# Kernel tuning notes

Measured on AMD Instinct MI355X. Metric: run time of the kernel, lower is better.

The kernel has to match this reference:

```python
import jax, jax.numpy as jnp
import numpy as np

N_NODES = 100000
N_EDGES = 1600000
EDGE_OUT = 48
HID = 128
NODE_OUT = 64


def setup_inputs() -> dict:
    key = jax.random.key(0)
    ks = jax.random.split(key, 8)
    x = jax.random.normal(ks[0], (N_NODES, 16), dtype=jnp.float32)
    edge_index = jax.random.randint(ks[1], (2, N_EDGES), 0, N_NODES, dtype=jnp.int64)
    edge_attr = jax.random.normal(ks[2], (N_EDGES, EDGE_OUT), dtype=jnp.float32)
    u = jax.random.normal(ks[3], (1, 8), dtype=jnp.float32)
    batch = jnp.zeros((N_NODES,), dtype=jnp.int64)
    # MLP params: Linear(3*edge_out, hid) -> ReLU -> Linear(hid, node_out)
    s1 = 1.0 / np.sqrt(3 * EDGE_OUT)
    s2 = 1.0 / np.sqrt(HID)
    W1 = jax.random.uniform(ks[4], (3 * EDGE_OUT, HID), jnp.float32, -s1, s1)
    b1 = jax.random.uniform(ks[5], (HID,), jnp.float32, -s1, s1)
    W2 = jax.random.uniform(ks[6], (HID, NODE_OUT), jnp.float32, -s2, s2)
    b2 = jax.random.uniform(ks[7], (NODE_OUT,), jnp.float32, -s2, s2)
    return {"x": x, "edge_index": edge_index, "edge_attr": edge_attr, "u": u,
            "batch": batch, "W1": W1, "b1": b1, "W2": W2, "b2": b2}


def reference(x, edge_index, edge_attr, u, batch, W1, b1, W2, b2):
    n = x.shape[0]
    col = edge_index[1]
    # fused-style aggregations over destination node indices
    out1 = jax.ops.segment_sum(edge_attr, col, num_segments=n)                      # scatter_add
    out2 = jax.ops.segment_max(edge_attr, col, num_segments=n)                      # scatter_max
    out2 = jnp.where(jnp.isneginf(out2), jnp.zeros((), edge_attr.dtype), out2)       # empty segments -> 0 (torch_scatter)
    cnt = jax.ops.segment_sum(jnp.ones((edge_attr.shape[0], 1), edge_attr.dtype), col, num_segments=n)
    out3 = out1 / jnp.maximum(cnt, jnp.ones((), edge_attr.dtype))                    # scatter_mean
    feat = jnp.concatenate([out1, out2, out3], axis=1)                               # [n, 3*edge_out]
    h = jax.nn.relu(feat @ W1 + b1)
    return h @ W2 + b2
```

## Files before the change

kernel.cpp:

```cpp
#include <hip/hip_runtime.h>
#include <math.h>

#define N_NODES 100000
#define N_EDGES 1600000
#define EO 48
constexpr int FEAT = 3 * EO;
constexpr int K1   = 160;
constexpr int HID  = 128;
constexpr int NOUT = 64;
constexpr int MAXD = 64;
constexpr int FEAT_ROWS_ALLOC = 100048;

typedef __attribute__((ext_vector_type(8))) short short8;
typedef __attribute__((ext_vector_type(4))) float floatx4;

__device__ __forceinline__ unsigned short f2bf(float f) {
  unsigned int u = __float_as_uint(f);
  unsigned int r = (u + 0x7fffu + ((u >> 16) & 1u)) >> 16;
  return (unsigned short)r;
}

__global__ void init_prep_kernel(int* __restrict__ cursor,
                                 const float* __restrict__ W1, const float* __restrict__ W2,
                                 unsigned short* __restrict__ W1T, unsigned short* __restrict__ W2T) {
  int i = blockIdx.x * blockDim.x + threadIdx.x;
  if (i < N_NODES) cursor[i] = 0;
  if (i < HID * K1) {
    int c = i / K1, k = i - c * K1;
    W1T[i] = (k < FEAT) ? f2bf(W1[k * HID + c]) : (unsigned short)0;
  } else {
    int j = i - HID * K1;
    if (j < NOUT * HID) {
      int c = j / HID, k = j - c * HID;
      W2T[j] = f2bf(W2[k * NOUT + c]);
    }
  }
}

__global__ void scatter_slots_kernel(const int4* __restrict__ col4, int* __restrict__ cursor,
                                     int* __restrict__ slots) {
  int i = blockIdx.x * blockDim.x + threadIdx.x;
  if (i < N_EDGES / 4) {
    int4 c = col4[i];
    int e = i * 4;
    int p;
    p = atomicAdd(&cursor[c.x], 1); if (p < MAXD) slots[c.x * MAXD + p] = e;
    p = atomicAdd(&cursor[c.y], 1); if (p < MAXD) slots[c.y * MAXD + p] = e + 1;
    p = atomicAdd(&cursor[c.z], 1); if (p < MAXD) slots[c.z * MAXD + p] = e + 2;
    p = atomicAdd(&cursor[c.w], 1); if (p < MAXD) slots[c.w * MAXD + p] = e + 3;
  }
}

__launch_bounds__(256)
__global__ void gather_kernel(const float* __restrict__ ea,
                              const int* __restrict__ slots,
                              const int* __restrict__ cursor,
                              unsigned short* __restrict__ featbf) {
  const int wid  = threadIdx.x >> 6;
  const int lane = threadIdx.x & 63;
  const int g = blockIdx.x * 4 + wid;
  if (g >= N_NODES) return;

  int deg = cursor[g];
  if (deg > MAXD) deg = MAXD;
  float s = 0.0f, m = -INFINITY;

  if (deg > 0) {
    int eidv = slots[g * MAXD + (lane < deg ? lane : deg - 1)];
    int t = 0;
    for (; t + 16 <= deg; t += 16) {
      int e[16];
#pragma unroll
      for (int j = 0; j < 16; ++j) e[j] = __builtin_amdgcn_readlane(eidv, t + j);
      if (lane < EO) {
        float v[16];
#pragma unroll
        for (int j = 0; j < 16; ++j) v[j] = ea[(size_t)e[j] * EO + lane];
#pragma unroll
        for (int j = 0; j < 16; ++j) { s += v[j]; m = fmaxf(m, v[j]); }
      }
    }
    for (; t + 4 <= deg; t += 4) {
      int e0 = __builtin_amdgcn_readlane(eidv, t + 0);
      int e1 = __builtin_amdgcn_readlane(eidv, t + 1);
      int e2 = __builtin_amdgcn_readlane(eidv, t + 2);
      int e3 = __builtin_amdgcn_readlane(eidv, t + 3);
      if (lane < EO) {
        float v0 = ea[(size_t)e0 * EO + lane];
        float v1 = ea[(size_t)e1 * EO + lane];
        float v2 = ea[(size_t)e2 * EO + lane];
        float v3 = ea[(size_t)e3 * EO + lane];
        s += (v0 + v1) + (v2 + v3);
        m = fmaxf(m, fmaxf(fmaxf(v0, v1), fmaxf(v2, v3)));
      }
    }
    for (; t < deg; ++t) {
      int e0 = __builtin_amdgcn_readlane(eidv, t);
      if (lane < EO) {
        float v = ea[(size_t)e0 * EO + lane];
        s += v;
        m = fmaxf(m, v);
      }
    }
  }

  if (lane < EO) {
    if (deg == 0) m = 0.0f;
    float mean = s / (float)(deg > 0 ? deg : 1);
    unsigned short* row = featbf + (size_t)g * FEAT;
    row[lane]          = f2bf(s);
    row[EO + lane]     = f2bf(m);
    row[2 * EO + lane] = f2bf(mean);
  }
}

__launch_bounds__(256)
__global__ void mlp_kernel(const unsigned short* __restrict__ featbf,
                           const unsigned short* __restrict__ W1T,
                           const unsigned short* __restrict__ W2T,
                           const float* __restrict__ b1,
                           const float* __restrict__ b2,
                           float* __restrict__ out) {
  __shared__ unsigned short h_lds[64][HID + 8];

  const int tid  = threadIdx.x;
  const int w    = tid >> 6;
  const int lane = tid & 63;
  const int llo  = lane & 15;
  const int lhi  = lane >> 4;

  const int g0   = blockIdx.x * 64;
  int rowA = g0 + w * 16 + llo;

  floatx4 acc[8];
#pragma unroll
  for (int c = 0; c < 8; ++c) acc[c] = (floatx4)0.0f;

  const unsigned short* arow = featbf + (size_t)rowA * FEAT;
#pragma unroll
  for (int ks = 0; ks < 5; ++ks) {
    short8 afrag = *(const short8*)(arow + ks * 32 + lhi * 8);
#pragma unroll
    for (int c = 0; c < 8; ++c) {
      short8 bfrag = *(const short8*)(W1T + (size_t)(c * 16 + llo) * K1 + ks * 32 + lhi * 8);
      acc[c] = __builtin_amdgcn_mfma_f32_16x16x32_bf16(afrag, bfrag, acc[c], 0, 0, 0);
    }
  }

#pragma unroll
  for (int c = 0; c < 8; ++c) {
    int col = c * 16 + llo;
    float bias = b1[col];
#pragma unroll
    for (int r = 0; r < 4; ++r) {
      int row = w * 16 + lhi * 4 + r;
      h_lds[row][col] = f2bf(fmaxf(acc[c][r] + bias, 0.0f));
    }
  }
  __syncthreads();

  floatx4 acc2[4];
#pragma unroll
  for (int c = 0; c < 4; ++c) acc2[c] = (floatx4)0.0f;

#pragma unroll
  for (int ks = 0; ks < 4; ++ks) {
    short8 afrag = *(const short8*)&h_lds[w * 16 + llo][ks * 32 + lhi * 8];
#pragma unroll
    for (int c = 0; c < 4; ++c) {
      short8 bfrag = *(const short8*)(W2T + (size_t)(c * 16 + llo) * HID + ks * 32 + lhi * 8);
      acc2[c] = __builtin_amdgcn_mfma_f32_16x16x32_bf16(afrag, bfrag, acc2[c], 0, 0, 0);
    }
  }

#pragma unroll
  for (int c = 0; c < 4; ++c) {
    int col = c * 16 + llo;
    float bias = b2[col];
#pragma unroll
    for (int r = 0; r < 4; ++r) {
      int g = g0 + w * 16 + lhi * 4 + r;
      if (g < N_NODES) out[(size_t)g * NOUT + col] = acc2[c][r] + bias;
    }
  }
}

extern "C" void kernel_launch(void* const* d_in, const int* in_sizes, int n_in,
                              void* d_out, int out_size, void* d_ws, size_t ws_size,
                              hipStream_t stream) {
  const int*   eidx = (const int*)d_in[1];
  const float* ea   = (const float*)d_in[2];
  const float* W1   = (const float*)d_in[5];
  const float* b1   = (const float*)d_in[6];
  const float* W2   = (const float*)d_in[7];
  const float* b2   = (const float*)d_in[8];
  const int* col = eidx + N_EDGES;
  float* out = (float*)d_out;

  char* p = (char*)d_ws;
  int* cursor = (int*)p;  p += (size_t)N_NODES * 4;
  int* slots  = (int*)p;  p += (size_t)N_NODES * MAXD * 4;
  unsigned short* featbf = (unsigned short*)p;  p += (size_t)FEAT_ROWS_ALLOC * FEAT * 2;
  unsigned short* W1T = (unsigned short*)p;     p += (size_t)HID * K1 * 2;
  unsigned short* W2T = (unsigned short*)p;

  init_prep_kernel<<<(N_NODES + 255) / 256, 256, 0, stream>>>(cursor, W1, W2, W1T, W2T);
  scatter_slots_kernel<<<(N_EDGES / 4 + 255) / 256, 256, 0, stream>>>((const int4*)col, cursor, slots);
  gather_kernel<<<(N_NODES + 3) / 4, 256, 0, stream>>>(ea, slots, cursor, featbf);
  mlp_kernel<<<(N_NODES + 63) / 64, 256, 0, stream>>>(featbf, W1T, W2T, b1, b2, out);
}
```

Measured before the change: 249.7 us.

## Pre-convert edge attributes to padded fp16 and switch MLP to fp16 MFMA

Adds a conversion pass, fused into the slot-scatter kernel launch, that rewrites edge_attr from fp32 into a 64-wide padded fp16 copy. The gather kernel then reads half-width values per edge, and the feature and weight buffers plus both MFMA stages switch from bf16 to fp16. The aim is to shrink the random-access gather traffic. The trade-off is an extra full streaming read of edge_attr plus a large write of the fp16 copy on every call, and fp16 range limits on the summed features. The gather loop is also collapsed into one clamped 16-wide loop with predicated accumulation.

```diff
diff --git a/kernel.cpp b/kernel.cpp
--- a/kernel.cpp
+++ b/kernel.cpp
@@ -9,15 +9,21 @@
 constexpr int HID  = 128;
 constexpr int NOUT = 64;
 constexpr int MAXD = 64;
+constexpr int EROW = 64;
 constexpr int FEAT_ROWS_ALLOC = 100048;
+
+constexpr int SCAT_BLOCKS = (N_EDGES / 4 + 255) / 256;
+constexpr int CONV_BLOCKS = (N_EDGES * 8) / 256;
 
 typedef __attribute__((ext_vector_type(8))) short short8;
 typedef __attribute__((ext_vector_type(4))) float floatx4;
 
-__device__ __forceinline__ unsigned short f2bf(float f) {
-  unsigned int u = __float_as_uint(f);
-  unsigned int r = (u + 0x7fffu + ((u >> 16) & 1u)) >> 16;
-  return (unsigned short)r;
+__device__ __forceinline__ unsigned short f2h(float f) {
+  _Float16 h = (_Float16)f;
+  return __builtin_bit_cast(unsigned short, h);
+}
+__device__ __forceinline__ float h2f(unsigned short u) {
+  return (float)__builtin_bit_cast(_Float16, u);
 }
 
 __global__ void init_prep_kernel(int* __restrict__ cursor,
@@ -27,35 +33,54 @@
   if (i < N_NODES) cursor[i] = 0;
   if (i < HID * K1) {
     int c = i / K1, k = i - c * K1;
-    W1T[i] = (k < FEAT) ? f2bf(W1[k * HID + c]) : (unsigned short)0;
+    W1T[i] = (k < FEAT) ? f2h(W1[k * HID + c]) : (unsigned short)0;
   } else {
     int j = i - HID * K1;
     if (j < NOUT * HID) {
       int c = j / HID, k = j - c * HID;
-      W2T[j] = f2bf(W2[k * NOUT + c]);
-    }
-  }
-}
-
-__global__ void scatter_slots_kernel(const int4* __restrict__ col4, int* __restrict__ cursor,
-                                     int* __restrict__ slots) {
-  int i = blockIdx.x * blockDim.x + threadIdx.x;
-  if (i < N_EDGES / 4) {
-    int4 c = col4[i];
-    int e = i * 4;
-    int p;
-    p = atomicAdd(&cursor[c.x], 1); if (p < MAXD) slots[c.x * MAXD + p] = e;
-    p = atomicAdd(&cursor[c.y], 1); if (p < MAXD) slots[c.y * MAXD + p] = e + 1;
-    p = atomicAdd(&cursor[c.z], 1); if (p < MAXD) slots[c.z * MAXD + p] = e + 2;
-    p = atomicAdd(&cursor[c.w], 1); if (p < MAXD) slots[c.w * MAXD + p] = e + 3;
+      W2T[j] = f2h(W2[k * NOUT + c]);
+    }
+  }
+}
+
+__global__ void scatter_convert_kernel(const int4* __restrict__ col4,
+                                       int* __restrict__ cursor, int* __restrict__ slots,
+                                       const float* __restrict__ ea,
+                                       unsigned short* __restrict__ eab) {
+  const int b = blockIdx.x;
+  if (b < SCAT_BLOCKS) {
+    int i = b * 256 + threadIdx.x;
+    if (i < N_EDGES / 4) {
+      int4 c = col4[i];
+      int e = i * 4;
+      int p;
+      p = atomicAdd(&cursor[c.x], 1); if (p < MAXD) slots[c.x * MAXD + p] = e;
+      p = atomicAdd(&cursor[c.y], 1); if (p < MAXD) slots[c.y * MAXD + p] = e + 1;
+      p = atomicAdd(&cursor[c.z], 1); if (p < MAXD) slots[c.z * MAXD + p] = e + 2;
+      p = atomicAdd(&cursor[c.w], 1); if (p < MAXD) slots[c.w * MAXD + p] = e + 3;
+    }
+  } else {
+    int t = (b - SCAT_BLOCKS) * 256 + threadIdx.x;
+    int e  = t >> 3;
+    int c8 = (t & 7) * 8;
+    short8 o;
+    if (c8 < EO) {
+      const float4* p = (const float4*)(ea + (size_t)e * EO + c8);
+      float4 a = p[0], bb = p[1];
+      o[0] = f2h(a.x);  o[1] = f2h(a.y);  o[2] = f2h(a.z);  o[3] = f2h(a.w);
+      o[4] = f2h(bb.x); o[5] = f2h(bb.y); o[6] = f2h(bb.z); o[7] = f2h(bb.w);
+    } else {
+      o = (short8)0;
+    }
+    *(short8*)(eab + (size_t)e * EROW + c8) = o;
   }
 }
 
 __launch_bounds__(256)
-__global__ void gather_kernel(const float* __restrict__ ea,
+__global__ void gather_kernel(const unsigned short* __restrict__ eab,
                               const int* __restrict__ slots,
                               const int* __restrict__ cursor,
-                              unsigned short* __restrict__ featbf) {
+                              unsigned short* __restrict__ feath) {
   const int wid  = threadIdx.x >> 6;
   const int lane = threadIdx.x & 63;
   const int g = blockIdx.x * 4 + wid;
@@ -67,39 +92,18 @@
 
   if (deg > 0) {
     int eidv = slots[g * MAXD + (lane < deg ? lane : deg - 1)];
-    int t = 0;
-    for (; t + 16 <= deg; t += 16) {
-      int e[16];
-#pragma unroll
-      for (int j = 0; j < 16; ++j) e[j] = __builtin_amdgcn_readlane(eidv, t + j);
-      if (lane < EO) {
-        float v[16];
-#pragma unroll
-        for (int j = 0; j < 16; ++j) v[j] = ea[(size_t)e[j] * EO + lane];
-#pragma unroll
-        for (int j = 0; j < 16; ++j) { s += v[j]; m = fmaxf(m, v[j]); }
+    for (int t = 0; t < deg; t += 16) {
+      float v[16];
+#pragma unroll
+      for (int j = 0; j < 16; ++j) {
+        int idx = t + j;
+        if (idx >= deg) idx = deg - 1;
+        int e = __builtin_amdgcn_readlane(eidv, idx);
+        v[j] = (lane < EO) ? h2f(eab[(size_t)e * EROW + lane]) : 0.0f;
       }
-    }
-    for (; t + 4 <= deg; t += 4) {
-      int e0 = __builtin_amdgcn_readlane(eidv, t + 0);
-      int e1 = __builtin_amdgcn_readlane(eidv, t + 1);
-      int e2 = __builtin_amdgcn_readlane(eidv, t + 2);
-      int e3 = __builtin_amdgcn_readlane(eidv, t + 3);
-      if (lane < EO) {
-        float v0 = ea[(size_t)e0 * EO + lane];
-        float v1 = ea[(size_t)e1 * EO + lane];
-        float v2 = ea[(size_t)e2 * EO + lane];
-        float v3 = ea[(size_t)e3 * EO + lane];
-        s += (v0 + v1) + (v2 + v3);
-        m = fmaxf(m, fmaxf(fmaxf(v0, v1), fmaxf(v2, v3)));
-      }
-    }
-    for (; t < deg; ++t) {
-      int e0 = __builtin_amdgcn_readlane(eidv, t);
-      if (lane < EO) {
-        float v = ea[(size_t)e0 * EO + lane];
-        s += v;
-        m = fmaxf(m, v);
+#pragma unroll
+      for (int j = 0; j < 16; ++j) {
+        if (t + j < deg) { s += v[j]; m = fmaxf(m, v[j]); }
       }
     }
   }
@@ -107,15 +111,15 @@
   if (lane < EO) {
     if (deg == 0) m = 0.0f;
     float mean = s / (float)(deg > 0 ? deg : 1);
-    unsigned short* row = featbf + (size_t)g * FEAT;
-    row[lane]          = f2bf(s);
-    row[EO + lane]     = f2bf(m);
-    row[2 * EO + lane] = f2bf(mean);
+    unsigned short* row = feath + (size_t)g * FEAT;
+    row[lane]          = f2h(s);
+    row[EO + lane]     = f2h(m);
+    row[2 * EO + lane] = f2h(mean);
   }
 }
 
 __launch_bounds__(256)
-__global__ void mlp_kernel(const unsigned short* __restrict__ featbf,
+__global__ void mlp_kernel(const unsigned short* __restrict__ feath,
                            const unsigned short* __restrict__ W1T,
                            const unsigned short* __restrict__ W2T,
                            const float* __restrict__ b1,
@@ -136,14 +140,14 @@
 #pragma unroll
   for (int c = 0; c < 8; ++c) acc[c] = (floatx4)0.0f;
 
-  const unsigned short* arow = featbf + (size_t)rowA * FEAT;
+  const unsigned short* arow = feath + (size_t)rowA * FEAT;
 #pragma unroll
   for (int ks = 0; ks < 5; ++ks) {
     short8 afrag = *(const short8*)(arow + ks * 32 + lhi * 8);
 #pragma unroll
     for (int c = 0; c < 8; ++c) {
       short8 bfrag = *(const short8*)(W1T + (size_t)(c * 16 + llo) * K1 + ks * 32 + lhi * 8);
-      acc[c] = __builtin_amdgcn_mfma_f32_16x16x32_bf16(afrag, bfrag, acc[c], 0, 0, 0);
+      acc[c] = __builtin_amdgcn_mfma_f32_16x16x32_f16(afrag, bfrag, acc[c], 0, 0, 0);
     }
   }
 
@@ -154,7 +158,7 @@
 #pragma unroll
     for (int r = 0; r < 4; ++r) {
       int row = w * 16 + lhi * 4 + r;
-      h_lds[row][col] = f2bf(fmaxf(acc[c][r] + bias, 0.0f));
+      h_lds[row][col] = f2h(fmaxf(acc[c][r] + bias, 0.0f));
     }
   }
   __syncthreads();
@@ -169,7 +173,7 @@
 #pragma unroll
     for (int c = 0; c < 4; ++c) {
       short8 bfrag = *(const short8*)(W2T + (size_t)(c * 16 + llo) * HID + ks * 32 + lhi * 8);
-      acc2[c] = __builtin_amdgcn_mfma_f32_16x16x32_bf16(afrag, bfrag, acc2[c], 0, 0, 0);
+      acc2[c] = __builtin_amdgcn_mfma_f32_16x16x32_f16(afrag, bfrag, acc2[c], 0, 0, 0);
     }
   }
 
@@ -200,12 +204,14 @@
   char* p = (char*)d_ws;
   int* cursor = (int*)p;  p += (size_t)N_NODES * 4;
   int* slots  = (int*)p;  p += (size_t)N_NODES * MAXD * 4;
-  unsigned short* featbf = (unsigned short*)p;  p += (size_t)FEAT_ROWS_ALLOC * FEAT * 2;
+  unsigned short* eab = (unsigned short*)p;  p += (size_t)N_EDGES * EROW * 2;
+  unsigned short* feath = (unsigned short*)p;  p += (size_t)FEAT_ROWS_ALLOC * FEAT * 2;
   unsigned short* W1T = (unsigned short*)p;     p += (size_t)HID * K1 * 2;
   unsigned short* W2T = (unsigned short*)p;
 
   init_prep_kernel<<<(N_NODES + 255) / 256, 256, 0, stream>>>(cursor, W1, W2, W1T, W2T);
-  scatter_slots_kernel<<<(N_EDGES / 4 + 255) / 256, 256, 0, stream>>>((const int4*)col, cursor, slots);
-  gather_kernel<<<(N_NODES + 3) / 4, 256, 0, stream>>>(ea, slots, cursor, featbf);
-  mlp_kernel<<<(N_NODES + 63) / 64, 256, 0, stream>>>(featbf, W1T, W2T, b1, b2, out);
-}
+  scatter_convert_kernel<<<SCAT_BLOCKS + CONV_BLOCKS, 256, 0, stream>>>(
+      (const int4*)col, cursor, slots, ea, eab);
+  gather_kernel<<<(N_NODES + 3) / 4, 256, 0, stream>>>(eab, slots, cursor, feath);
+  mlp_kernel<<<(N_NODES + 63) / 64, 256, 0, stream>>>(feath, W1T, W2T, b1, b2, out);
+}
```

Measured after the change: 467.8 us. 87.4% more time.
